# Kernel tuning notes

Measured on AMD Instinct MI355X. Metric: run time of the kernel, lower is better.

## Reference

```python
import jax, jax.numpy as jnp
import numpy as np
from jax import lax

B, T, I, H = 64, 512, 256, 256


def setup_inputs() -> dict:
    key = jax.random.key(0)
    ks = jax.random.split(key, 5)
    s_in = 1.0 / np.sqrt(I)
    s_h = 1.0 / np.sqrt(H)
    return {
        "x": jax.random.normal(ks[0], (B, T, I), dtype=jnp.float32),
        "W0": jax.random.normal(ks[1], (I, 4 * H), dtype=jnp.float32) * s_in,
        "U0": jax.random.normal(ks[2], (H, 4 * H), dtype=jnp.float32) * s_h,
        "b0": jnp.zeros((4 * H,), dtype=jnp.float32),
        "W1": jax.random.normal(ks[3], (H, 4 * H), dtype=jnp.float32) * s_h,
        "U1": jax.random.normal(ks[4], (H, 4 * H), dtype=jnp.float32) * s_h,
        "b1": jnp.zeros((4 * H,), dtype=jnp.float32),
    }


def _lstm_layer(x, W, U, b):
    # x: [B, T, Din]; W: [Din, 4H]; U: [H, 4H]; b: [4H]
    h_dim = U.shape[0]
    batch = x.shape[0]
    # Precompute input projections for all timesteps in one GEMM.
    xz = jnp.einsum('bti,ig->btg', x, W) + b  # [B, T, 4H]

    def step(carry, xzt):
        h, c = carry
        z = xzt + h @ U  # [B, 4H]
        i, f, g, o = jnp.split(z, 4, axis=-1)
        c = jax.nn.sigmoid(f) * c + jax.nn.sigmoid(i) * jnp.tanh(g)
        h = jax.nn.sigmoid(o) * jnp.tanh(c)
        return (h, c), h

    init = (jnp.zeros((batch, h_dim), x.dtype), jnp.zeros((batch, h_dim), x.dtype))
    _, hs = lax.scan(step, init, jnp.swapaxes(xz, 0, 1))  # hs: [T, B, H]
    return jnp.swapaxes(hs, 0, 1)  # [B, T, H]


def reference(x, W0, U0, b0, W1, U1, b1):
    y = _lstm_layer(x, W0, U0, b0)
    y = _lstm_layer(y, W1, U1, b1)
    return y
```

## Files before the change

kernel.cpp:

```cpp
#include <hip/hip_runtime.h>

typedef unsigned short ushort_t;
typedef unsigned int uint_t;

using f16x8 = __attribute__((ext_vector_type(8))) _Float16;
using f32x4 = __attribute__((ext_vector_type(4))) float;
using u32x4 = __attribute__((ext_vector_type(4))) unsigned int;

#define BATCH 64
#define SEQT 512
#define DIN 256
#define HID 256
#define G4 1024
#define CH 32
#define NCH (SEQT / CH)

static __device__ __forceinline__ ushort_t f16b(float x) {
    return __builtin_bit_cast(ushort_t, (_Float16)x);
}
static __device__ __forceinline__ float f16f(ushort_t u) {
    return (float)__builtin_bit_cast(_Float16, u);
}
static __device__ __forceinline__ uint_t pk2(float a, float b) {
    return (uint_t)f16b(a) | ((uint_t)f16b(b) << 16);
}
static __device__ __forceinline__ float sig_(float x) {
    return 1.f / (1.f + __expf(-x));
}
static __device__ __forceinline__ float tanh_(float x) {
    float e = __expf(2.f * x);
    return (e - 1.f) / (e + 1.f);
}

#define PINA(x) asm volatile("" : "+a"(x))
#define PINV(x) asm volatile("" : "+v"(x))

static __device__ __forceinline__ f16x8 asf16(u32x4 v) {
    return __builtin_bit_cast(f16x8, v);
}


__global__ void cvt_x_kernel(const float* __restrict__ in, ushort_t* __restrict__ out, int n4) {
    int i = blockIdx.x * blockDim.x + threadIdx.x;
    if (i < n4) {
        float4 v = ((const float4*)in)[i];
        ushort4 o;
        o.x = f16b(v.x); o.y = f16b(v.y); o.z = f16b(v.z); o.w = f16b(v.w);
        ((ushort4*)out)[i] = o;
    }
}

__global__ void prep_wt_kernel(const float* __restrict__ W, ushort_t* __restrict__ Wt) {
    int tid = blockIdx.x * blockDim.x + threadIdx.x;
    int k = tid >> 10;
    int n = tid & 1023;
    Wt[n * DIN + k] = f16b(W[tid]);
}

__global__ void prep_upk_kernel(const float* __restrict__ U, uint4* __restrict__ Upk) {
    int tid = blockIdx.x * blockDim.x + threadIdx.x;
    int j = tid >> 10;
    int g = tid & 1023;
    uint4 o;
    uint_t* op = &o.x;
#pragma unroll
    for (int q = 0; q < 4; ++q) {
        float a = U[(8 * j + 2 * q) * G4 + g];
        float b = U[(8 * j + 2 * q + 1) * G4 + g];
        op[q] = pk2(a, b);
    }
    Upk[tid] = o;
}


#define GSTRIDE 40

__global__ __launch_bounds__(256) void gemm_f16_kernel(
    const ushort_t* __restrict__ A,
    const ushort_t* __restrict__ Bt,
    const float* __restrict__ bias,
    ushort_t* __restrict__ C,
    int M)
{
    const int K = DIN, N = G4;
    __shared__ ushort_t As[128 * GSTRIDE];
    __shared__ ushort_t Bs[128 * GSTRIDE];
    int tid = threadIdx.x;
    int bx = blockIdx.x & 7;
    int by = blockIdx.x >> 3;
    int m0 = by * 128, n0 = bx * 128;
    int w = tid >> 6, lane = tid & 63;
    int wr = (w >> 1) * 64, wc = (w & 1) * 64;
    int r = lane & 15, kg = lane >> 4;

    f32x4 acc[4][4];
#pragma unroll
    for (int i = 0; i < 4; ++i)
#pragma unroll
        for (int j = 0; j < 4; ++j)
            acc[i][j] = f32x4{0.f, 0.f, 0.f, 0.f};

    for (int kt = 0; kt < K; kt += 32) {
        __syncthreads();
#pragma unroll
        for (int s = 0; s < 2; ++s) {
            int chunk = tid + s * 256;
            int row = chunk >> 2;
            int ko = (chunk & 3) * 8;
            uint4 va = *(const uint4*)(A + (size_t)(m0 + row) * K + kt + ko);
            *(uint4*)(&As[row * GSTRIDE + ko]) = va;
            uint4 vb = *(const uint4*)(Bt + (size_t)(n0 + row) * K + kt + ko);
            *(uint4*)(&Bs[row * GSTRIDE + ko]) = vb;
        }
        __syncthreads();
        f16x8 af[4], bf[4];
#pragma unroll
        for (int i = 0; i < 4; ++i) {
            af[i] = *(const f16x8*)(&As[(wr + i * 16 + r) * GSTRIDE + kg * 8]);
            bf[i] = *(const f16x8*)(&Bs[(wc + i * 16 + r) * GSTRIDE + kg * 8]);
        }
#pragma unroll
        for (int i = 0; i < 4; ++i)
#pragma unroll
            for (int j = 0; j < 4; ++j)
                acc[i][j] = __builtin_amdgcn_mfma_f32_16x16x32_f16(af[i], bf[j], acc[i][j], 0, 0, 0);
    }

#pragma unroll
    for (int i = 0; i < 4; ++i)
#pragma unroll
        for (int j = 0; j < 4; ++j) {
            int col = n0 + wc + j * 16 + r;
            float bv = bias[col];
#pragma unroll
            for (int v = 0; v < 4; ++v) {
                int rowg = m0 + wr + i * 16 + kg * 4 + v;
                C[(size_t)rowg * N + col] = f16b(acc[i][j][v] + bv);
            }
        }
}


__global__ __launch_bounds__(256)
__attribute__((amdgpu_waves_per_eu(1, 1)))
void lstm_pipe3_kernel(
    const ushort_t* __restrict__ xz1h,
    const u32x4* __restrict__ Upk0,
    const u32x4* __restrict__ Upk1,
    const ushort_t* __restrict__ Wt1,
    const float* __restrict__ b1,
    uint_t* y1pk,
    int* flag1, int* flag2, int* flag3,
    uint_t* xz2u,
    float* __restrict__ out,
    int T)
{
    __shared__ __align__(16) u32x4 Uld[4][2][16][64];
    __shared__ __align__(16) ushort_t ys[32][264];
    __shared__ __align__(16) ushort_t h16[2][HID];

    const int tid = threadIdx.x;
    const int w = tid >> 6;
    const int l = tid & 63;
    const int lg = l >> 4;
    const int lr = l & 15;
    const int role = (int)(blockIdx.x >> 6);
    const int b = (int)(blockIdx.x & 63);
    const int hcol = w * 64 + lg * 16 + lr;

    int* f1p = flag1 + b * 32;
    int* f2p = flag2 + b * 32;
    int* f3p = flag3 + b * 32;

    if (role == 1) {
        float b1w[16];
#pragma unroll
        for (int ct = 0; ct < 16; ++ct) b1w[ct] = b1[(w * 16 + ct) * 16 + lr];
        __syncthreads();

        for (int ch = 0; ch < NCH; ++ch) {
            if (tid == 0) {
                while (__hip_atomic_load(f1p, __ATOMIC_ACQUIRE, __HIP_MEMORY_SCOPE_AGENT) < ch + 1)
                    __builtin_amdgcn_s_sleep(32);
                while (__hip_atomic_load(f3p, __ATOMIC_ACQUIRE, __HIP_MEMORY_SCOPE_AGENT) < ch - 3)
                    __builtin_amdgcn_s_sleep(32);
            }
            __syncthreads();

#pragma unroll
            for (int it = 0; it < 16; ++it) {
                int idx = it * 256 + tid;
                int row = idx >> 7;
                int j = idx & 127;
                uint_t v = __hip_atomic_load(
                    &y1pk[(size_t)(b * T + ch * CH + row) * 128 + j],
                    __ATOMIC_RELAXED, __HIP_MEMORY_SCOPE_AGENT);
                *(uint_t*)&ys[row][2 * j] = v;
            }
            __syncthreads();

            uint_t* xzbuf = xz2u + ((size_t)(b * 4 + (ch & 3)) * CH) * G4;
#pragma unroll
            for (int ct = 0; ct < 16; ++ct) {
                int ctI = w * 16 + ct;
                u32x4 bf[8];
#pragma unroll
                for (int kt = 0; kt < 8; ++kt)
                    bf[kt] = *(const u32x4*)(Wt1 + (size_t)(ctI * 16 + lr) * DIN + kt * 32 + lg * 8);
                f32x4 acc[2];
                acc[0] = f32x4{0.f, 0.f, 0.f, 0.f};
                acc[1] = f32x4{0.f, 0.f, 0.f, 0.f};
#pragma unroll
                for (int rt = 0; rt < 2; ++rt)
#pragma unroll
                    for (int kt = 0; kt < 8; ++kt) {
                        f16x8 af = *(const f16x8*)&ys[rt * 16 + lr][kt * 32 + lg * 8];
                        acc[rt] = __builtin_amdgcn_mfma_f32_16x16x32_f16(
                            af, asf16(bf[kt]), acc[rt], 0, 0, 0);
                    }
#pragma unroll
                for (int rt = 0; rt < 2; ++rt)
#pragma unroll
                    for (int v = 0; v < 4; ++v) {
                        int row = rt * 16 + lg * 4 + v;
                        float z = acc[rt][v] + b1w[ct];
                        __hip_atomic_store(&xzbuf[(size_t)row * G4 + ctI * 16 + lr],
                                           __builtin_bit_cast(uint_t, z),
                                           __ATOMIC_RELAXED, __HIP_MEMORY_SCOPE_AGENT);
                    }
            }
            __syncthreads();
            if (tid == 0)
                __hip_atomic_store(f2p, ch + 1, __ATOMIC_RELEASE, __HIP_MEMORY_SCOPE_AGENT);
        }
        return;
    }

    const u32x4* Upk = (role == 2) ? Upk1 : Upk0;
    u32x4 ua[64];
    u32x4 uv[32];
#pragma unroll
    for (int gb = 0; gb < 4; ++gb)
#pragma unroll
        for (int ti = 0; ti < 4; ++ti) {
            int col = (gb * 16 + w * 4 + ti) * 16 + lr;
            int fi = gb * 4 + ti;
#pragma unroll
            for (int kt = 0; kt < 4; ++kt)
                ua[fi * 4 + kt] = Upk[(kt * 4 + lg) * 1024 + col];
#pragma unroll
            for (int k2 = 0; k2 < 2; ++k2)
                uv[fi * 2 + k2] = Upk[((4 + k2) * 4 + lg) * 1024 + col];
        }
#pragma unroll
    for (int i = 0; i < 64; ++i) PINA(ua[i]);
#pragma unroll
    for (int i = 0; i < 32; ++i) PINV(uv[i]);

#pragma unroll
    for (int gb = 0; gb < 4; ++gb)
#pragma unroll
        for (int ti = 0; ti < 4; ++ti) {
            int col = (gb * 16 + w * 4 + ti) * 16 + lr;
            int fi = gb * 4 + ti;
#pragma unroll
            for (int k2 = 0; k2 < 2; ++k2)
                Uld[w][k2][fi][l] = Upk[((6 + k2) * 4 + lg) * 1024 + col];
        }

    h16[0][tid] = 0;
    float c = 0.f;

#define STEP_BODY(AF, XZC, ZG)                                                        \
    {                                                                                 \
        _Pragma("unroll")                                                             \
        for (int gb = 0; gb < 4; ++gb) {                                              \
            f32x4 accA[4], accB[4];                                                   \
            _Pragma("unroll")                                                         \
            for (int ti = 0; ti < 4; ++ti) {                                          \
                accA[ti] = f32x4{0.f, 0.f, 0.f, 0.f};                                 \
                accB[ti] = f32x4{0.f, 0.f, 0.f, 0.f};                                 \
            }                                                                         \
            _Pragma("unroll")                                                         \
            for (int ti = 0; ti < 4; ++ti) {                                          \
                int fi = gb * 4 + ti;                                                 \
                _Pragma("unroll")                                                     \
                for (int kt = 0; kt < 4; ++kt)                                        \
                    accA[ti] = __builtin_amdgcn_mfma_f32_16x16x32_f16(                \
                        AF[kt], asf16(ua[fi * 4 + kt]), accA[ti], 0, 0, 0);           \
                _Pragma("unroll")                                                     \
                for (int k2 = 0; k2 < 2; ++k2)                                        \
                    accB[ti] = __builtin_amdgcn_mfma_f32_16x16x32_f16(                \
                        AF[4 + k2], asf16(uv[fi * 2 + k2]), accB[ti], 0, 0, 0);       \
                _Pragma("unroll")                                                     \
                for (int k2 = 0; k2 < 2; ++k2) {                                      \
                    u32x4 ub = Uld[w][k2][fi][l];                                     \
                    accB[ti] = __builtin_amdgcn_mfma_f32_16x16x32_f16(                \
                        AF[6 + k2], asf16(ub), accB[ti], 0, 0, 0);                    \
                }                                                                     \
            }                                                                         \
            float za = (lg == 0) ? accA[0][0] : (lg == 1) ? accA[1][0]                \
                     : (lg == 2) ? accA[2][0] : accA[3][0];                           \
            float zb = (lg == 0) ? accB[0][0] : (lg == 1) ? accB[1][0]                \
                     : (lg == 2) ? accB[2][0] : accB[3][0];                           \
            ZG[gb] = za + zb + XZC[gb];                                               \
        }                                                                             \
    }

    if (role == 0) {
        uint_t* hr = (uint_t*)&ys[0][0];
        const ushort_t* xz_b = xz1h + (size_t)b * T * G4;
        float xzc[4];
#pragma unroll
        for (int gb = 0; gb < 4; ++gb) xzc[gb] = f16f(xz_b[gb * 256 + hcol]);
        __syncthreads();

        for (int t = 0; t < T; ++t) {
            const int cur = t & 1, nxt = cur ^ 1;

            f16x8 af[8];
#pragma unroll
            for (int kt = 0; kt < 8; ++kt)
                af[kt] = *(const f16x8*)((const char*)&h16[cur][0] + kt * 64 + lg * 16);

            float xzn[4];
            {
                const ushort_t* xztn = xz_b + (size_t)((t + 1 < T) ? (t + 1) : t) * G4;
#pragma unroll
                for (int gb = 0; gb < 4; ++gb) xzn[gb] = f16f(xztn[gb * 256 + hcol]);
            }

            float zg[4];
            STEP_BODY(af, xzc, zg);

            c = sig_(zg[1]) * c + sig_(zg[0]) * tanh_(zg[2]);
            float h = sig_(zg[3]) * tanh_(c);

            h16[nxt][hcol] = f16b(h);
            {
                uint_t hb = (uint_t)f16b(h);
                uint_t pb = (uint_t)(unsigned)__shfl_xor((int)hb, 1);
                if (!(l & 1))
                    hr[(t & (CH - 1)) * 128 + (hcol >> 1)] = hb | (pb << 16);
            }
#pragma unroll
            for (int gb = 0; gb < 4; ++gb) xzc[gb] = xzn[gb];

            __syncthreads();

            if ((t & (CH - 1)) == (CH - 1)) {
                int t0 = t - (CH - 1);
#pragma unroll
                for (int it = 0; it < 16; ++it) {
                    int idx = it * 256 + tid;
                    int row = idx >> 7;
                    int j = idx & 127;
                    __hip_atomic_store(&y1pk[(size_t)(b * T + t0 + row) * 128 + j],
                                       hr[row * 128 + j],
                                       __ATOMIC_RELAXED, __HIP_MEMORY_SCOPE_AGENT);
                }
                __syncthreads();
                if (tid == 0)
                    __hip_atomic_store(f1p, (t + 1) / CH, __ATOMIC_RELEASE,
                                       __HIP_MEMORY_SCOPE_AGENT);
            }
        }
    } else {
        size_t obase = (size_t)b * T * HID + hcol;
        __syncthreads();

        for (int ch = 0; ch < NCH; ++ch) {
            if (tid == 0) {
                while (__hip_atomic_load(f2p, __ATOMIC_ACQUIRE, __HIP_MEMORY_SCOPE_AGENT) < ch + 1)
                    __builtin_amdgcn_s_sleep(32);
            }
            __syncthreads();

            const uint_t* xzbuf = xz2u + ((size_t)(b * 4 + (ch & 3)) * CH) * G4;

            for (int tb = 0; tb < CH; ++tb) {
                const int t = ch * CH + tb;
                const int cur = t & 1, nxt = cur ^ 1;

                float xzc[4];
#pragma unroll
                for (int gb = 0; gb < 4; ++gb) {
                    uint_t u = __hip_atomic_load(&xzbuf[(size_t)tb * G4 + gb * 256 + hcol],
                                                 __ATOMIC_RELAXED, __HIP_MEMORY_SCOPE_AGENT);
                    xzc[gb] = __builtin_bit_cast(float, u);
                }

                f16x8 af[8];
#pragma unroll
                for (int kt = 0; kt < 8; ++kt)
                    af[kt] = *(const f16x8*)((const char*)&h16[cur][0] + kt * 64 + lg * 16);

                float zg[4];
                STEP_BODY(af, xzc, zg);

                c = sig_(zg[1]) * c + sig_(zg[0]) * tanh_(zg[2]);
                float h = sig_(zg[3]) * tanh_(c);

                h16[nxt][hcol] = f16b(h);
                out[obase] = h;
                obase += HID;

                __syncthreads();
            }
            if (tid == 0)
                __hip_atomic_store(f3p, ch + 1, __ATOMIC_RELEASE, __HIP_MEMORY_SCOPE_AGENT);
        }
    }
#undef STEP_BODY
}


extern "C" void kernel_launch(void* const* d_in, const int* in_sizes, int n_in,
                              void* d_out, int out_size, void* d_ws, size_t ws_size,
                              hipStream_t stream) {
    const float* x  = (const float*)d_in[0];
    const float* W0 = (const float*)d_in[1];
    const float* U0 = (const float*)d_in[2];
    const float* b0 = (const float*)d_in[3];
    const float* W1 = (const float*)d_in[4];
    const float* U1 = (const float*)d_in[5];
    const float* b1 = (const float*)d_in[6];
    float* out = (float*)d_out;

    const size_t M = (size_t)BATCH * SEQT;

    char* ws = (char*)d_ws;
    ushort_t* xf16  = (ushort_t*)(ws);
    uint_t*   y1pk  = (uint_t*)  (ws + (16u << 20));
    ushort_t* Wt0   = (ushort_t*)(ws + (32u << 20));
    ushort_t* Wt1   = (ushort_t*)(ws + (32u << 20) + 524288);
    u32x4*    Upk0  = (u32x4*)   (ws + (33u << 20));
    u32x4*    Upk1  = (u32x4*)   (ws + (33u << 20) + 524288);
    int*      flag1 = (int*)     (ws + (34u << 20));
    int*      flag2 = (int*)     (ws + (34u << 20) + 65536);
    int*      flag3 = (int*)     (ws + (34u << 20) + 131072);
    uint_t*   xz2u  = (uint_t*)  (ws + (35u << 20));
    ushort_t* xz1h  = (ushort_t*)(ws + (67u << 20));

    hipMemsetAsync(flag1, 0, 196608, stream);

    {
        int n4 = (int)(M * DIN / 4);
        cvt_x_kernel<<<dim3((n4 + 255) / 256), dim3(256), 0, stream>>>(x, xf16, n4);
        prep_wt_kernel<<<dim3(1024), dim3(256), 0, stream>>>(W0, Wt0);
        prep_wt_kernel<<<dim3(1024), dim3(256), 0, stream>>>(W1, Wt1);
        prep_upk_kernel<<<dim3(128), dim3(256), 0, stream>>>(U0, (uint4*)Upk0);
        prep_upk_kernel<<<dim3(128), dim3(256), 0, stream>>>(U1, (uint4*)Upk1);
    }

    gemm_f16_kernel<<<dim3((int)(M / 128) * 8), dim3(256), 0, stream>>>(xf16, Wt0, b0, xz1h, (int)M);

    lstm_pipe3_kernel<<<dim3(192), dim3(256), 0, stream>>>(
        xz1h, Upk0, Upk1, Wt1, b1, y1pk, flag1, flag2, flag3, xz2u, out, SEQT);
}
```

Baseline: 1.191 ms.

## Fold layer-0 input GEMM into persistent pipeline as fourth role; merge prep kernels

Removes the standalone layer-0 input-projection GEMM and adds a new producer role (64 more blocks) that computes each batch's xz chunk on the fly. It publishes the chunk to the layer-0 recurrence through a flag, so the projection overlaps the sequential recurrence instead of running before it. The chunk size is halved so producer and consumer stages hand off more finely, and the five prep kernels are merged into one launch to cut launch overhead. The cost is more flag polling and per-step global atomic loads of packed xz. The design also relies on all 256 blocks being co-resident, since blocks spin-wait on each other's flags.

```diff
diff --git a/kernel.cpp b/kernel.cpp
--- a/kernel.cpp
+++ b/kernel.cpp
@@ -12,7 +12,7 @@
 #define DIN 256
 #define HID 256
 #define G4 1024
-#define CH 32
+#define CH 16
 #define NCH (SEQT / CH)
 
 static __device__ __forceinline__ ushort_t f16b(float x) {
@@ -40,117 +40,61 @@
 }
 
 
-__global__ void cvt_x_kernel(const float* __restrict__ in, ushort_t* __restrict__ out, int n4) {
-    int i = blockIdx.x * blockDim.x + threadIdx.x;
-    if (i < n4) {
-        float4 v = ((const float4*)in)[i];
+__global__ void prep_all_kernel(
+    const float* __restrict__ x,
+    const float* __restrict__ W0, const float* __restrict__ W1,
+    const float* __restrict__ U0, const float* __restrict__ U1,
+    ushort_t* __restrict__ xf16,
+    ushort_t* __restrict__ Wt0, ushort_t* __restrict__ Wt1,
+    uint4* __restrict__ Upk0, uint4* __restrict__ Upk1)
+{
+    int blk = blockIdx.x;
+    int tid = threadIdx.x;
+    if (blk < 8192) {
+        int i = blk * 256 + tid;
+        float4 v = ((const float4*)x)[i];
         ushort4 o;
         o.x = f16b(v.x); o.y = f16b(v.y); o.z = f16b(v.z); o.w = f16b(v.w);
-        ((ushort4*)out)[i] = o;
+        ((ushort4*)xf16)[i] = o;
+    } else if (blk < 10240) {
+        const float* W = (blk < 9216) ? W0 : W1;
+        ushort_t* Wt = (blk < 9216) ? Wt0 : Wt1;
+        int t = ((blk - 8192) & 1023) * 256 + tid;
+        int k = t >> 10;
+        int n = t & 1023;
+        Wt[n * DIN + k] = f16b(W[t]);
+    } else {
+        const float* U = (blk < 10368) ? U0 : U1;
+        uint4* Upk = (blk < 10368) ? Upk0 : Upk1;
+        int t = ((blk - 10240) & 127) * 256 + tid;
+        int j = t >> 10;
+        int g = t & 1023;
+        uint4 o;
+        uint_t* op = &o.x;
+#pragma unroll
+        for (int q = 0; q < 4; ++q) {
+            float a = U[(8 * j + 2 * q) * G4 + g];
+            float bb = U[(8 * j + 2 * q + 1) * G4 + g];
+            op[q] = pk2(a, bb);
+        }
+        Upk[t] = o;
     }
-}
-
-__global__ void prep_wt_kernel(const float* __restrict__ W, ushort_t* __restrict__ Wt) {
-    int tid = blockIdx.x * blockDim.x + threadIdx.x;
-    int k = tid >> 10;
-    int n = tid & 1023;
-    Wt[n * DIN + k] = f16b(W[tid]);
-}
-
-__global__ void prep_upk_kernel(const float* __restrict__ U, uint4* __restrict__ Upk) {
-    int tid = blockIdx.x * blockDim.x + threadIdx.x;
-    int j = tid >> 10;
-    int g = tid & 1023;
-    uint4 o;
-    uint_t* op = &o.x;
-#pragma unroll
-    for (int q = 0; q < 4; ++q) {
-        float a = U[(8 * j + 2 * q) * G4 + g];
-        float b = U[(8 * j + 2 * q + 1) * G4 + g];
-        op[q] = pk2(a, b);
-    }
-    Upk[tid] = o;
-}
-
-
-#define GSTRIDE 40
-
-__global__ __launch_bounds__(256) void gemm_f16_kernel(
-    const ushort_t* __restrict__ A,
-    const ushort_t* __restrict__ Bt,
-    const float* __restrict__ bias,
-    ushort_t* __restrict__ C,
-    int M)
-{
-    const int K = DIN, N = G4;
-    __shared__ ushort_t As[128 * GSTRIDE];
-    __shared__ ushort_t Bs[128 * GSTRIDE];
-    int tid = threadIdx.x;
-    int bx = blockIdx.x & 7;
-    int by = blockIdx.x >> 3;
-    int m0 = by * 128, n0 = bx * 128;
-    int w = tid >> 6, lane = tid & 63;
-    int wr = (w >> 1) * 64, wc = (w & 1) * 64;
-    int r = lane & 15, kg = lane >> 4;
-
-    f32x4 acc[4][4];
-#pragma unroll
-    for (int i = 0; i < 4; ++i)
-#pragma unroll
-        for (int j = 0; j < 4; ++j)
-            acc[i][j] = f32x4{0.f, 0.f, 0.f, 0.f};
-
-    for (int kt = 0; kt < K; kt += 32) {
-        __syncthreads();
-#pragma unroll
-        for (int s = 0; s < 2; ++s) {
-            int chunk = tid + s * 256;
-            int row = chunk >> 2;
-            int ko = (chunk & 3) * 8;
-            uint4 va = *(const uint4*)(A + (size_t)(m0 + row) * K + kt + ko);
-            *(uint4*)(&As[row * GSTRIDE + ko]) = va;
-            uint4 vb = *(const uint4*)(Bt + (size_t)(n0 + row) * K + kt + ko);
-            *(uint4*)(&Bs[row * GSTRIDE + ko]) = vb;
-        }
-        __syncthreads();
-        f16x8 af[4], bf[4];
-#pragma unroll
-        for (int i = 0; i < 4; ++i) {
-            af[i] = *(const f16x8*)(&As[(wr + i * 16 + r) * GSTRIDE + kg * 8]);
-            bf[i] = *(const f16x8*)(&Bs[(wc + i * 16 + r) * GSTRIDE + kg * 8]);
-        }
-#pragma unroll
-        for (int i = 0; i < 4; ++i)
-#pragma unroll
-            for (int j = 0; j < 4; ++j)
-                acc[i][j] = __builtin_amdgcn_mfma_f32_16x16x32_f16(af[i], bf[j], acc[i][j], 0, 0, 0);
-    }
-
-#pragma unroll
-    for (int i = 0; i < 4; ++i)
-#pragma unroll
-        for (int j = 0; j < 4; ++j) {
-            int col = n0 + wc + j * 16 + r;
-            float bv = bias[col];
-#pragma unroll
-            for (int v = 0; v < 4; ++v) {
-                int rowg = m0 + wr + i * 16 + kg * 4 + v;
-                C[(size_t)rowg * N + col] = f16b(acc[i][j][v] + bv);
-            }
-        }
 }
 
 
 __global__ __launch_bounds__(256)
 __attribute__((amdgpu_waves_per_eu(1, 1)))
-void lstm_pipe3_kernel(
-    const ushort_t* __restrict__ xz1h,
+void lstm_pipe4_kernel(
+    const ushort_t* __restrict__ xf16,
     const u32x4* __restrict__ Upk0,
     const u32x4* __restrict__ Upk1,
+    const ushort_t* __restrict__ Wt0,
     const ushort_t* __restrict__ Wt1,
+    const float* __restrict__ b0,
     const float* __restrict__ b1,
+    uint_t* xz1u,
     uint_t* y1pk,
-    int* flag1, int* flag2, int* flag3,
+    int* flag0, int* flag1, int* flag2, int* flag3,
     uint_t* xz2u,
     float* __restrict__ out,
     int T)
@@ -168,15 +112,64 @@
     const int b = (int)(blockIdx.x & 63);
     const int hcol = w * 64 + lg * 16 + lr;
 
+    int* f0p = flag0 + b * 32;
     int* f1p = flag1 + b * 32;
     int* f2p = flag2 + b * 32;
     int* f3p = flag3 + b * 32;
 
-    if (role == 1) {
-        float b1w[16];
-#pragma unroll
-        for (int ct = 0; ct < 16; ++ct) b1w[ct] = b1[(w * 16 + ct) * 16 + lr];
-        __syncthreads();
+    if (role == 0) {
+        float bw[16];
+#pragma unroll
+        for (int ct = 0; ct < 16; ++ct) bw[ct] = b0[(w * 16 + ct) * 16 + lr];
+
+        for (int ch = 0; ch < NCH; ++ch) {
+            __syncthreads();
+#pragma unroll
+            for (int s = 0; s < 2; ++s) {
+                int u = tid * 2 + s;
+                int row = u >> 5;
+                int ko = (u & 31) * 8;
+                *(uint4*)&ys[row][ko] =
+                    *(const uint4*)(xf16 + (size_t)(b * T + ch * CH + row) * 256 + ko);
+            }
+            __syncthreads();
+#pragma unroll
+            for (int ct = 0; ct < 16; ++ct) {
+                int ctI = w * 16 + ct;
+                u32x4 bf[8];
+#pragma unroll
+                for (int kt = 0; kt < 8; ++kt)
+                    bf[kt] = *(const u32x4*)(Wt0 + (size_t)(ctI * 16 + lr) * DIN + kt * 32 + lg * 8);
+                f32x4 acc = f32x4{0.f, 0.f, 0.f, 0.f};
+#pragma unroll
+                for (int kt = 0; kt < 8; ++kt) {
+                    f16x8 af = *(const f16x8*)&ys[lr][kt * 32 + lg * 8];
+                    acc = __builtin_amdgcn_mfma_f32_16x16x32_f16(af, asf16(bf[kt]), acc, 0, 0, 0);
+                }
+#pragma unroll
+                for (int v = 0; v < 4; ++v) {
+                    float z = acc[v] + bw[ct];
+                    uint_t own = (uint_t)f16b(z);
+                    uint_t pb = (uint_t)(unsigned)__shfl_xor((int)own, 1);
+                    if (!(l & 1)) {
+                        size_t word = (size_t)(b * T + ch * CH + lg * 4 + v) * 512
+                                      + ctI * 8 + (lr >> 1);
+                        __hip_atomic_store(&xz1u[word], own | (pb << 16),
+                                           __ATOMIC_RELAXED, __HIP_MEMORY_SCOPE_AGENT);
+                    }
+                }
+            }
+            __syncthreads();
+            if (tid == 0)
+                __hip_atomic_store(f0p, ch + 1, __ATOMIC_RELEASE, __HIP_MEMORY_SCOPE_AGENT);
+        }
+        return;
+    }
+
+    if (role == 2) {
+        float bw[16];
+#pragma unroll
+        for (int ct = 0; ct < 16; ++ct) bw[ct] = b1[(w * 16 + ct) * 16 + lr];
 
         for (int ch = 0; ch < NCH; ++ch) {
             if (tid == 0) {
@@ -186,9 +179,8 @@
                     __builtin_amdgcn_s_sleep(32);
             }
             __syncthreads();
-
-#pragma unroll
-            for (int it = 0; it < 16; ++it) {
+#pragma unroll
+            for (int it = 0; it < 8; ++it) {
                 int idx = it * 256 + tid;
                 int row = idx >> 7;
                 int j = idx & 127;
@@ -207,27 +199,19 @@
 #pragma unroll
                 for (int kt = 0; kt < 8; ++kt)
                     bf[kt] = *(const u32x4*)(Wt1 + (size_t)(ctI * 16 + lr) * DIN + kt * 32 + lg * 8);
-                f32x4 acc[2];
-                acc[0] = f32x4{0.f, 0.f, 0.f, 0.f};
-                acc[1] = f32x4{0.f, 0.f, 0.f, 0.f};
-#pragma unroll
-                for (int rt = 0; rt < 2; ++rt)
-#pragma unroll
-                    for (int kt = 0; kt < 8; ++kt) {
-                        f16x8 af = *(const f16x8*)&ys[rt * 16 + lr][kt * 32 + lg * 8];
-                        acc[rt] = __builtin_amdgcn_mfma_f32_16x16x32_f16(
-                            af, asf16(bf[kt]), acc[rt], 0, 0, 0);
-                    }
-#pragma unroll
-                for (int rt = 0; rt < 2; ++rt)
-#pragma unroll
-                    for (int v = 0; v < 4; ++v) {
-                        int row = rt * 16 + lg * 4 + v;
-                        float z = acc[rt][v] + b1w[ct];
-                        __hip_atomic_store(&xzbuf[(size_t)row * G4 + ctI * 16 + lr],
-                                           __builtin_bit_cast(uint_t, z),
-                                           __ATOMIC_RELAXED, __HIP_MEMORY_SCOPE_AGENT);
-                    }
+                f32x4 acc = f32x4{0.f, 0.f, 0.f, 0.f};
+#pragma unroll
+                for (int kt = 0; kt < 8; ++kt) {
+                    f16x8 af = *(const f16x8*)&ys[lr][kt * 32 + lg * 8];
+                    acc = __builtin_amdgcn_mfma_f32_16x16x32_f16(af, asf16(bf[kt]), acc, 0, 0, 0);
+                }
+#pragma unroll
+                for (int v = 0; v < 4; ++v) {
+                    float z = acc[v] + bw[ct];
+                    __hip_atomic_store(&xzbuf[(size_t)(lg * 4 + v) * G4 + ctI * 16 + lr],
+                                       __builtin_bit_cast(uint_t, z),
+                                       __ATOMIC_RELAXED, __HIP_MEMORY_SCOPE_AGENT);
+                }
             }
             __syncthreads();
             if (tid == 0)
@@ -236,7 +220,7 @@
         return;
     }
 
-    const u32x4* Upk = (role == 2) ? Upk1 : Upk0;
+    const u32x4* Upk = (role == 3) ? Upk1 : Upk0;
     u32x4 ua[64];
     u32x4 uv[32];
 #pragma unroll
@@ -307,27 +291,49 @@
         }                                                                             \
     }
 
-    if (role == 0) {
+    if (role == 1) {
         uint_t* hr = (uint_t*)&ys[0][0];
-        const ushort_t* xz_b = xz1h + (size_t)b * T * G4;
-        float xzc[4];
-#pragma unroll
-        for (int gb = 0; gb < 4; ++gb) xzc[gb] = f16f(xz_b[gb * 256 + hcol]);
+        uint_t xzw[4], xzn[4];
         __syncthreads();
 
         for (int t = 0; t < T; ++t) {
             const int cur = t & 1, nxt = cur ^ 1;
 
+            if ((t & (CH - 1)) == 0) {
+                if (tid == 0) {
+                    while (__hip_atomic_load(f0p, __ATOMIC_ACQUIRE, __HIP_MEMORY_SCOPE_AGENT)
+                           < t / CH + 1)
+                        __builtin_amdgcn_s_sleep(16);
+                }
+                __syncthreads();
+#pragma unroll
+                for (int gb = 0; gb < 4; ++gb)
+                    xzw[gb] = __hip_atomic_load(
+                        &xz1u[(size_t)(b * T + t) * 512 + ((gb * 256 + hcol) >> 1)],
+                        __ATOMIC_RELAXED, __HIP_MEMORY_SCOPE_AGENT);
+            } else {
+#pragma unroll
+                for (int gb = 0; gb < 4; ++gb) xzw[gb] = xzn[gb];
+            }
+
             f16x8 af[8];
 #pragma unroll
             for (int kt = 0; kt < 8; ++kt)
                 af[kt] = *(const f16x8*)((const char*)&h16[cur][0] + kt * 64 + lg * 16);
 
-            float xzn[4];
-            {
-                const ushort_t* xztn = xz_b + (size_t)((t + 1 < T) ? (t + 1) : t) * G4;
-#pragma unroll
-                for (int gb = 0; gb < 4; ++gb) xzn[gb] = f16f(xztn[gb * 256 + hcol]);
+            if (t + 1 < T && ((t + 1) & (CH - 1)) != 0) {
+#pragma unroll
+                for (int gb = 0; gb < 4; ++gb)
+                    xzn[gb] = __hip_atomic_load(
+                        &xz1u[(size_t)(b * T + t + 1) * 512 + ((gb * 256 + hcol) >> 1)],
+                        __ATOMIC_RELAXED, __HIP_MEMORY_SCOPE_AGENT);
+            }
+
+            float xzc[4];
+#pragma unroll
+            for (int gb = 0; gb < 4; ++gb) {
+                uint_t u = xzw[gb];
+                xzc[gb] = f16f((ushort_t)((hcol & 1) ? (u >> 16) : (u & 0xffff)));
             }
 
             float zg[4];
@@ -343,15 +349,13 @@
                 if (!(l & 1))
                     hr[(t & (CH - 1)) * 128 + (hcol >> 1)] = hb | (pb << 16);
             }
-#pragma unroll
-            for (int gb = 0; gb < 4; ++gb) xzc[gb] = xzn[gb];
 
             __syncthreads();
 
             if ((t & (CH - 1)) == (CH - 1)) {
                 int t0 = t - (CH - 1);
 #pragma unroll
-                for (int it = 0; it < 16; ++it) {
+                for (int it = 0; it < 8; ++it) {
                     int idx = it * 256 + tid;
                     int row = idx >> 7;
                     int j = idx & 127;
@@ -427,8 +431,6 @@
     const float* b1 = (const float*)d_in[6];
     float* out = (float*)d_out;
 
-    const size_t M = (size_t)BATCH * SEQT;
-
     char* ws = (char*)d_ws;
     ushort_t* xf16  = (ushort_t*)(ws);
     uint_t*   y1pk  = (uint_t*)  (ws + (16u << 20));
@@ -436,25 +438,19 @@
     ushort_t* Wt1   = (ushort_t*)(ws + (32u << 20) + 524288);
     u32x4*    Upk0  = (u32x4*)   (ws + (33u << 20));
     u32x4*    Upk1  = (u32x4*)   (ws + (33u << 20) + 524288);
-    int*      flag1 = (int*)     (ws + (34u << 20));
-    int*      flag2 = (int*)     (ws + (34u << 20) + 65536);
-    int*      flag3 = (int*)     (ws + (34u << 20) + 131072);
+    int*      flag0 = (int*)     (ws + (34u << 20));
+    int*      flag1 = (int*)     (ws + (34u << 20) + 65536);
+    int*      flag2 = (int*)     (ws + (34u << 20) + 131072);
+    int*      flag3 = (int*)     (ws + (34u << 20) + 196608);
     uint_t*   xz2u  = (uint_t*)  (ws + (35u << 20));
-    ushort_t* xz1h  = (ushort_t*)(ws + (67u << 20));
-
-    hipMemsetAsync(flag1, 0, 196608, stream);
-
-    {
-        int n4 = (int)(M * DIN / 4);
-        cvt_x_kernel<<<dim3((n4 + 255) / 256), dim3(256), 0, stream>>>(x, xf16, n4);
-        prep_wt_kernel<<<dim3(1024), dim3(256), 0, stream>>>(W0, Wt0);
-        prep_wt_kernel<<<dim3(1024), dim3(256), 0, stream>>>(W1, Wt1);
-        prep_upk_kernel<<<dim3(128), dim3(256), 0, stream>>>(U0, (uint4*)Upk0);
-        prep_upk_kernel<<<dim3(128), dim3(256), 0, stream>>>(U1, (uint4*)Upk1);
-    }
-
-    gemm_f16_kernel<<<dim3((int)(M / 128) * 8), dim3(256), 0, stream>>>(xf16, Wt0, b0, xz1h, (int)M);
-
-    lstm_pipe3_kernel<<<dim3(192), dim3(256), 0, stream>>>(
-        xz1h, Upk0, Upk1, Wt1, b1, y1pk, flag1, flag2, flag3, xz2u, out, SEQT);
-}
+    uint_t*   xz1u  = (uint_t*)  (ws + (51u << 20));
+
+    hipMemsetAsync(flag0, 0, 262144, stream);
+
+    prep_all_kernel<<<dim3(10496), dim3(256), 0, stream>>>(
+        x, W0, W1, U0, U1, xf16, Wt0, Wt1, (uint4*)Upk0, (uint4*)Upk1);
+
+    lstm_pipe4_kernel<<<dim3(256), dim3(256), 0, stream>>>(
+        xf16, Upk0, Upk1, Wt0, Wt1, b0, b1,
+        xz1u, y1pk, flag0, flag1, flag2, flag3, xz2u, out, SEQT);
+}
```

Measured after the change: 1.305 ms. 1.1x slower.

## Halve pipeline chunk size, prefetch layer-2 xz, stage output, merge prep kernels

Applied to the files above, without the earlier changes.

Drops the chunk length that hands data between the layer-1 recurrence, the layer-2 input-projection GEMM and the layer-2 recurrence from 32 to 16 timesteps. The pipeline fills sooner, at the cost of more flag synchronisations. The layer-2 recurrence now prefetches the next timestep's gate inputs one step ahead and buffers h in shared memory, then writes each chunk out with coalesced stores instead of issuing scattered per-step global writes. The five preprocessing launches are merged into a single kernel to cut launch overhead.

```diff
diff --git a/kernel.cpp b/kernel.cpp
--- a/kernel.cpp
+++ b/kernel.cpp
@@ -12,7 +12,7 @@
 #define DIN 256
 #define HID 256
 #define G4 1024
-#define CH 32
+#define CH 16
 #define NCH (SEQT / CH)
 
 static __device__ __forceinline__ ushort_t f16b(float x) {
@@ -40,36 +40,45 @@
 }
 
 
-__global__ void cvt_x_kernel(const float* __restrict__ in, ushort_t* __restrict__ out, int n4) {
-    int i = blockIdx.x * blockDim.x + threadIdx.x;
-    if (i < n4) {
-        float4 v = ((const float4*)in)[i];
+__global__ void prep_all_kernel(
+    const float* __restrict__ x,
+    const float* __restrict__ W0, const float* __restrict__ W1,
+    const float* __restrict__ U0, const float* __restrict__ U1,
+    ushort_t* __restrict__ xf16,
+    ushort_t* __restrict__ Wt0, ushort_t* __restrict__ Wt1,
+    uint4* __restrict__ Upk0, uint4* __restrict__ Upk1)
+{
+    int blk = blockIdx.x;
+    int tid = threadIdx.x;
+    if (blk < 8192) {
+        int i = blk * 256 + tid;
+        float4 v = ((const float4*)x)[i];
         ushort4 o;
         o.x = f16b(v.x); o.y = f16b(v.y); o.z = f16b(v.z); o.w = f16b(v.w);
-        ((ushort4*)out)[i] = o;
+        ((ushort4*)xf16)[i] = o;
+    } else if (blk < 10240) {
+        const float* W = (blk < 9216) ? W0 : W1;
+        ushort_t* Wt = (blk < 9216) ? Wt0 : Wt1;
+        int t = ((blk - 8192) & 1023) * 256 + tid;
+        int k = t >> 10;
+        int n = t & 1023;
+        Wt[n * DIN + k] = f16b(W[t]);
+    } else {
+        const float* U = (blk < 10368) ? U0 : U1;
+        uint4* Upk = (blk < 10368) ? Upk0 : Upk1;
+        int t = ((blk - 10240) & 127) * 256 + tid;
+        int j = t >> 10;
+        int g = t & 1023;
+        uint4 o;
+        uint_t* op = &o.x;
+#pragma unroll
+        for (int q = 0; q < 4; ++q) {
+            float a = U[(8 * j + 2 * q) * G4 + g];
+            float bb = U[(8 * j + 2 * q + 1) * G4 + g];
+            op[q] = pk2(a, bb);
+        }
+        Upk[t] = o;
     }
-}
-
-__global__ void prep_wt_kernel(const float* __restrict__ W, ushort_t* __restrict__ Wt) {
-    int tid = blockIdx.x * blockDim.x + threadIdx.x;
-    int k = tid >> 10;
-    int n = tid & 1023;
-    Wt[n * DIN + k] = f16b(W[tid]);
-}
-
-__global__ void prep_upk_kernel(const float* __restrict__ U, uint4* __restrict__ Upk) {
-    int tid = blockIdx.x * blockDim.x + threadIdx.x;
-    int j = tid >> 10;
-    int g = tid & 1023;
-    uint4 o;
-    uint_t* op = &o.x;
-#pragma unroll
-    for (int q = 0; q < 4; ++q) {
-        float a = U[(8 * j + 2 * q) * G4 + g];
-        float b = U[(8 * j + 2 * q + 1) * G4 + g];
-        op[q] = pk2(a, b);
-    }
-    Upk[tid] = o;
 }
 
 
@@ -188,7 +197,7 @@
             __syncthreads();
 
 #pragma unroll
-            for (int it = 0; it < 16; ++it) {
+            for (int it = 0; it < 8; ++it) {
                 int idx = it * 256 + tid;
                 int row = idx >> 7;
                 int j = idx & 127;
@@ -207,27 +216,19 @@
 #pragma unroll
                 for (int kt = 0; kt < 8; ++kt)
                     bf[kt] = *(const u32x4*)(Wt1 + (size_t)(ctI * 16 + lr) * DIN + kt * 32 + lg * 8);
-                f32x4 acc[2];
-                acc[0] = f32x4{0.f, 0.f, 0.f, 0.f};
-                acc[1] = f32x4{0.f, 0.f, 0.f, 0.f};
-#pragma unroll
-                for (int rt = 0; rt < 2; ++rt)
-#pragma unroll
-                    for (int kt = 0; kt < 8; ++kt) {
-                        f16x8 af = *(const f16x8*)&ys[rt * 16 + lr][kt * 32 + lg * 8];
-                        acc[rt] = __builtin_amdgcn_mfma_f32_16x16x32_f16(
-                            af, asf16(bf[kt]), acc[rt], 0, 0, 0);
-                    }
-#pragma unroll
-                for (int rt = 0; rt < 2; ++rt)
-#pragma unroll
-                    for (int v = 0; v < 4; ++v) {
-                        int row = rt * 16 + lg * 4 + v;
-                        float z = acc[rt][v] + b1w[ct];
-                        __hip_atomic_store(&xzbuf[(size_t)row * G4 + ctI * 16 + lr],
-                                           __builtin_bit_cast(uint_t, z),
-                                           __ATOMIC_RELAXED, __HIP_MEMORY_SCOPE_AGENT);
-                    }
+                f32x4 acc = f32x4{0.f, 0.f, 0.f, 0.f};
+#pragma unroll
+                for (int kt = 0; kt < 8; ++kt) {
+                    f16x8 af = *(const f16x8*)&ys[lr][kt * 32 + lg * 8];
+                    acc = __builtin_amdgcn_mfma_f32_16x16x32_f16(af, asf16(bf[kt]), acc, 0, 0, 0);
+                }
+#pragma unroll
+                for (int v = 0; v < 4; ++v) {
+                    float z = acc[v] + b1w[ct];
+                    __hip_atomic_store(&xzbuf[(size_t)(lg * 4 + v) * G4 + ctI * 16 + lr],
+                                       __builtin_bit_cast(uint_t, z),
+                                       __ATOMIC_RELAXED, __HIP_MEMORY_SCOPE_AGENT);
+                }
             }
             __syncthreads();
             if (tid == 0)
@@ -351,7 +352,7 @@
             if ((t & (CH - 1)) == (CH - 1)) {
                 int t0 = t - (CH - 1);
 #pragma unroll
-                for (int it = 0; it < 16; ++it) {
+                for (int it = 0; it < 8; ++it) {
                     int idx = it * 256 + tid;
                     int row = idx >> 7;
                     int j = idx & 127;
@@ -366,7 +367,7 @@
             }
         }
     } else {
-        size_t obase = (size_t)b * T * HID + hcol;
+        float* orb = (float*)&ys[0][0];
         __syncthreads();
 
         for (int ch = 0; ch < NCH; ++ch) {
@@ -377,17 +378,20 @@
             __syncthreads();
 
             const uint_t* xzbuf = xz2u + ((size_t)(b * 4 + (ch & 3)) * CH) * G4;
+            uint_t xzw[4], xznw[4];
 
             for (int tb = 0; tb < CH; ++tb) {
                 const int t = ch * CH + tb;
                 const int cur = t & 1, nxt = cur ^ 1;
 
-                float xzc[4];
-#pragma unroll
-                for (int gb = 0; gb < 4; ++gb) {
-                    uint_t u = __hip_atomic_load(&xzbuf[(size_t)tb * G4 + gb * 256 + hcol],
-                                                 __ATOMIC_RELAXED, __HIP_MEMORY_SCOPE_AGENT);
-                    xzc[gb] = __builtin_bit_cast(float, u);
+                if (tb == 0) {
+#pragma unroll
+                    for (int gb = 0; gb < 4; ++gb)
+                        xzw[gb] = __hip_atomic_load(&xzbuf[gb * 256 + hcol],
+                                                    __ATOMIC_RELAXED, __HIP_MEMORY_SCOPE_AGENT);
+                } else {
+#pragma unroll
+                    for (int gb = 0; gb < 4; ++gb) xzw[gb] = xznw[gb];
                 }
 
                 f16x8 af[8];
@@ -395,6 +399,19 @@
                 for (int kt = 0; kt < 8; ++kt)
                     af[kt] = *(const f16x8*)((const char*)&h16[cur][0] + kt * 64 + lg * 16);
 
+                if (tb + 1 < CH) {
+#pragma unroll
+                    for (int gb = 0; gb < 4; ++gb)
+                        xznw[gb] = __hip_atomic_load(
+                            &xzbuf[(size_t)(tb + 1) * G4 + gb * 256 + hcol],
+                            __ATOMIC_RELAXED, __HIP_MEMORY_SCOPE_AGENT);
+                }
+
+                float xzc[4];
+#pragma unroll
+                for (int gb = 0; gb < 4; ++gb)
+                    xzc[gb] = __builtin_bit_cast(float, xzw[gb]);
+
                 float zg[4];
                 STEP_BODY(af, xzc, zg);
 
@@ -402,10 +419,17 @@
                 float h = sig_(zg[3]) * tanh_(c);
 
                 h16[nxt][hcol] = f16b(h);
-                out[obase] = h;
-                obase += HID;
+                orb[tb * 256 + hcol] = h;
 
                 __syncthreads();
+            }
+
+#pragma unroll
+            for (int it = 0; it < 16; ++it) {
+                int idx = it * 256 + tid;
+                int row = idx >> 8;
+                int col = idx & 255;
+                out[(size_t)(b * T + ch * CH + row) * HID + col] = orb[row * 256 + col];
             }
             if (tid == 0)
                 __hip_atomic_store(f3p, ch + 1, __ATOMIC_RELEASE, __HIP_MEMORY_SCOPE_AGENT);
@@ -440,18 +464,12 @@
     int*      flag2 = (int*)     (ws + (34u << 20) + 65536);
     int*      flag3 = (int*)     (ws + (34u << 20) + 131072);
     uint_t*   xz2u  = (uint_t*)  (ws + (35u << 20));
-    ushort_t* xz1h  = (ushort_t*)(ws + (67u << 20));
+    ushort_t* xz1h  = (ushort_t*)(ws + (51u << 20));
 
     hipMemsetAsync(flag1, 0, 196608, stream);
 
-    {
-        int n4 = (int)(M * DIN / 4);
-        cvt_x_kernel<<<dim3((n4 + 255) / 256), dim3(256), 0, stream>>>(x, xf16, n4);
-        prep_wt_kernel<<<dim3(1024), dim3(256), 0, stream>>>(W0, Wt0);
-        prep_wt_kernel<<<dim3(1024), dim3(256), 0, stream>>>(W1, Wt1);
-        prep_upk_kernel<<<dim3(128), dim3(256), 0, stream>>>(U0, (uint4*)Upk0);
-        prep_upk_kernel<<<dim3(128), dim3(256), 0, stream>>>(U1, (uint4*)Upk1);
-    }
+    prep_all_kernel<<<dim3(10496), dim3(256), 0, stream>>>(
+        x, W0, W1, U0, U1, xf16, Wt0, Wt1, (uint4*)Upk0, (uint4*)Upk1);
 
     gemm_f16_kernel<<<dim3((int)(M / 128) * 8), dim3(256), 0, stream>>>(xf16, Wt0, b0, xz1h, (int)M);
 
```

Result: faster. 1.120 ms, median of 2 (-5.9%).
